# Optimization experiments

Measured on AMD Instinct MI355X. Metric: run time of the kernel, lower is better.

Reference implementation:

```python
import jax, jax.numpy as jnp
import numpy as np

DIM = 384
WS = 8        # window_size
SHIFT = 4     # shift_size
HEADS = 8
HEAD_DIM = DIM // HEADS
SCALE = HEAD_DIM ** (-0.5)
EPS = 1e-5


def layernorm(x, g, b):
    m = jnp.mean(x, axis=-1, keepdims=True)
    v = jnp.var(x, axis=-1, keepdims=True)
    return (x - m) * jax.lax.rsqrt(v + EPS) * g + b


def setup_inputs() -> dict:
    key = jax.random.key(0)
    ks = jax.random.split(key, 8)
    s = 0.02
    return {
        "x": jax.random.normal(ks[0], (8, DIM, 64, 64), dtype=jnp.float32),
        "qkv_w": jax.random.normal(ks[1], (DIM, 3 * DIM), dtype=jnp.float32) * s,
        "qkv_b": jnp.zeros((3 * DIM,), jnp.float32),
        "proj_w": jax.random.normal(ks[2], (DIM, DIM), dtype=jnp.float32) * s,
        "proj_b": jnp.zeros((DIM,), jnp.float32),
        "ln1_g": jnp.ones((DIM,), jnp.float32),
        "ln1_b": jnp.zeros((DIM,), jnp.float32),
        "ln2_g": jnp.ones((DIM,), jnp.float32),
        "ln2_b": jnp.zeros((DIM,), jnp.float32),
        "mlp_w1": jax.random.normal(ks[3], (DIM, 4 * DIM), dtype=jnp.float32) * s,
        "mlp_b1": jnp.zeros((4 * DIM,), jnp.float32),
        "mlp_w2": jax.random.normal(ks[4], (4 * DIM, DIM), dtype=jnp.float32) * s,
        "mlp_b2": jnp.zeros((DIM,), jnp.float32),
    }


def reference(x, qkv_w, qkv_b, proj_w, proj_b, ln1_g, ln1_b, ln2_g, ln2_b,
              mlp_w1, mlp_b1, mlp_w2, mlp_b2):
    B, C, H, W = x.shape
    x_skip = jnp.transpose(x, (0, 2, 3, 1))  # [B,H,W,C]
    xh = x_skip
    pad_b = (-H) % WS
    pad_r = (-W) % WS
    xh = jnp.pad(xh, ((0, 0), (0, pad_b), (0, pad_r), (0, 0)))
    Hp, Wp = xh.shape[1], xh.shape[2]
    if SHIFT > 0:
        xh = jnp.roll(xh, (-SHIFT, -SHIFT), axis=(1, 2))
    # window partition -> [B*nH*nW, WS*WS, C]
    win = xh.reshape(B, Hp // WS, WS, Wp // WS, WS, C)
    win = win.transpose(0, 1, 3, 2, 4, 5).reshape(-1, WS * WS, C)
    win = layernorm(win, ln1_g, ln1_b)
    # windowed MHA (no shift mask in original module)
    Bw, N, _ = win.shape
    qkv = (win @ qkv_w + qkv_b).reshape(Bw, N, 3, HEADS, HEAD_DIM)
    qkv = qkv.transpose(2, 0, 3, 1, 4)  # [3, Bw, H, N, d]
    q, k, v = qkv[0] * SCALE, qkv[1], qkv[2]
    attn = jax.nn.softmax(jnp.einsum('bhnd,bhmd->bhnm', q, k), axis=-1)
    out = jnp.einsum('bhnm,bhmd->bhnd', attn, v)
    out = out.transpose(0, 2, 1, 3).reshape(Bw, N, C)
    out = out @ proj_w + proj_b
    # window reverse
    xh = out.reshape(B, Hp // WS, Wp // WS, WS, WS, C)
    xh = xh.transpose(0, 1, 3, 2, 4, 5).reshape(B, Hp, Wp, C)
    if SHIFT > 0:
        xh = jnp.roll(xh, (SHIFT, SHIFT), axis=(1, 2))
    xh = xh[:, :H, :W, :] + x_skip
    h = layernorm(xh, ln2_g, ln2_b)
    h = jax.nn.gelu(h @ mlp_w1 + mlp_b1, approximate=False) @ mlp_w2 + mlp_b2
    return jnp.transpose(h, (0, 3, 1, 2))  # [B,C,H,W]
```

## Files before the change

### kernel.cpp

```cpp
#include <hip/hip_runtime.h>
#include <hip/hip_bf16.h>
#include <math.h>

#define DIM   384
#define HEADS 8
#define HD    48
#define NTOK  32768
#define NWIN  512

typedef __attribute__((ext_vector_type(8))) short bf16x8;
typedef __attribute__((ext_vector_type(8))) unsigned short u16x8;
typedef __attribute__((ext_vector_type(4))) float f32x4;

__device__ __forceinline__ float bf2f(unsigned short u) {
    unsigned int v = ((unsigned int)u) << 16;
    return __uint_as_float(v);
}
__device__ __forceinline__ unsigned short f2bf(float f) {
    unsigned int x = __float_as_uint(f);
    unsigned int r = (x + 0x7fffu + ((x >> 16) & 1u)) >> 16;
    return (unsigned short)r;
}

__device__ __forceinline__ float gelu(float v) {
    float z  = v * 0.70710678118654752f;
    float az = fabsf(z);
    float t  = __builtin_amdgcn_rcpf(1.0f + 0.47047f * az);
    float p  = t * (0.3480242f + t * (-0.0958798f + t * 0.7478556f));
    float ea = 1.0f - p * __expf(-az * az);
    float er = copysignf(ea, z);
    return 0.5f * v * (1.0f + er);
}

__device__ __forceinline__ void tok2src(int tok, int& b, int& hs, int& ws) {
    int bb  = tok >> 12;
    int win = (tok >> 6) & 63;
    int t   = tok & 63;
    int hi = win >> 3, wi = win & 7;
    int r  = t >> 3,  cc = t & 7;
    b  = bb;
    hs = (hi * 8 + r  + 4) & 63;
    ws = (wi * 8 + cc + 4) & 63;
}

__global__ __launch_bounds__(256) void k_wt4(const float* __restrict__ qkv_w,
                                             const float* __restrict__ proj_w,
                                             const float* __restrict__ w1,
                                             const float* __restrict__ w2,
                                             unsigned short* __restrict__ d0,
                                             unsigned short* __restrict__ d1,
                                             unsigned short* __restrict__ d2,
                                             unsigned short* __restrict__ d3) {
    int idx = blockIdx.x * 256 + threadIdx.x;
    const float* W; unsigned short* Wt; int K, N, loc;
    if (idx < 442368)       { W = qkv_w;  Wt = d0; K = 384;  N = 1152; loc = idx; }
    else if (idx < 589824)  { W = proj_w; Wt = d1; K = 384;  N = 384;  loc = idx - 442368; }
    else if (idx < 1179648) { W = w1;     Wt = d2; K = 384;  N = 1536; loc = idx - 589824; }
    else                    { W = w2;     Wt = d3; K = 1536; N = 384;  loc = idx - 1179648; }
    int n = loc / K, k = loc - n * K;
    Wt[loc] = f2bf(W[(size_t)k * N + n]);
}

__global__ __launch_bounds__(256) void k_ln1(const float* __restrict__ x,
                                             const float* __restrict__ g,
                                             const float* __restrict__ bt,
                                             unsigned short* __restrict__ ln1) {
    int blk = blockIdx.x;
    int b  = blk >> 6, hs = blk & 63;
    int t  = threadIdx.x;
    int w  = t & 63, cg = t >> 6;
    const float* row = x + (size_t)b * DIM * 4096 + hs * 64;

    float sum = 0.f, sq = 0.f;
    for (int i = 0; i < 96; i++) {
        int c = i * 4 + cg;
        float v = row[(size_t)c * 4096 + w];
        sum += v; sq += v * v;
    }
    __shared__ float red[2][4][64];
    __shared__ float mean_s[64], rstd_s[64];
    red[0][cg][w] = sum; red[1][cg][w] = sq;
    __syncthreads();
    if (t < 64) {
        float s  = red[0][0][t] + red[0][1][t] + red[0][2][t] + red[0][3][t];
        float q2 = red[1][0][t] + red[1][1][t] + red[1][2][t] + red[1][3][t];
        float mean = s * (1.0f / DIM);
        float var  = q2 * (1.0f / DIM) - mean * mean;
        mean_s[t] = mean;
        rstd_s[t] = rsqrtf(var + 1e-5f);
    }
    __syncthreads();

    int wp = t >> 2, seg = t & 3;
    int hr = (hs + 60) & 63, wr = (wp + 60) & 63;
    int tok = ((b * 8 + (hr >> 3)) * 8 + (wr >> 3)) * 64 + (hr & 7) * 8 + (wr & 7);

    __shared__ __align__(16) unsigned short tile[64][72];
    for (int chunk = 0; chunk < 6; chunk++) {
        float mean = mean_s[w], rstd = rstd_s[w];
        #pragma unroll
        for (int it = 0; it < 16; it++) {
            int cl = it * 4 + cg;
            int c  = chunk * 64 + cl;
            float v = row[(size_t)c * 4096 + w];
            tile[w][cl] = f2bf((v - mean) * rstd * g[c] + bt[c]);
        }
        __syncthreads();
        u16x8 v0 = *(const u16x8*)&tile[wp][seg * 16];
        u16x8 v1 = *(const u16x8*)&tile[wp][seg * 16 + 8];
        unsigned short* op = ln1 + (size_t)tok * DIM + chunk * 64 + seg * 16;
        *(u16x8*)op = v0;
        *(u16x8*)(op + 8) = v1;
        __syncthreads();
    }
}

template <int EPI>
__global__ __launch_bounds__(256) void k_gemm_mfma(
        const unsigned short* __restrict__ A,
        const unsigned short* __restrict__ Bt,
        const float* __restrict__ bias,
        void* __restrict__ Cout,
        const float* __restrict__ xres,
        int N, int K, int GX) {
    __shared__ __align__(16) unsigned short SH[24576];
    int tid  = threadIdx.x;
    int lane = tid & 63;
    int wave = tid >> 6;
    int wm = wave >> 1, wn = wave & 1;
    int quad = lane >> 4, l15 = lane & 15;

    int l   = blockIdx.x;
    int xcd = l & 7;
    int r_  = l >> 3;
    int bx  = r_ % GX;
    int by  = (r_ / GX) * 8 + xcd;
    int m0 = by * 128, n0 = bx * 128;

    const unsigned short* gA0 = A  + (size_t)(m0 +      lane) * K + wave * 8;
    const unsigned short* gA1 = A  + (size_t)(m0 + 64 + lane) * K + wave * 8;
    const unsigned short* gB0 = Bt + (size_t)(n0 +      lane) * K + wave * 8;
    const unsigned short* gB1 = Bt + (size_t)(n0 + 64 + lane) * K + wave * 8;

    auto stage = [&](int buf) {
        __builtin_amdgcn_global_load_lds(
            (const __attribute__((address_space(1))) void*)gA0,
            (__attribute__((address_space(3))) void*)&SH[buf * 4096 + wave * 1024],
            16, 0, 0);
        __builtin_amdgcn_global_load_lds(
            (const __attribute__((address_space(1))) void*)gA1,
            (__attribute__((address_space(3))) void*)&SH[buf * 4096 + wave * 1024 + 512],
            16, 0, 0);
        __builtin_amdgcn_global_load_lds(
            (const __attribute__((address_space(1))) void*)gB0,
            (__attribute__((address_space(3))) void*)&SH[12288 + buf * 4096 + wave * 1024],
            16, 0, 0);
        __builtin_amdgcn_global_load_lds(
            (const __attribute__((address_space(1))) void*)gB1,
            (__attribute__((address_space(3))) void*)&SH[12288 + buf * 4096 + wave * 1024 + 512],
            16, 0, 0);
        gA0 += 32; gA1 += 32; gB0 += 32; gB1 += 32;
    };

    f32x4 acc[4][4] = {};
    int nsteps = K >> 5;

    stage(0);
    stage(1);
    int cur = 0, nxt = 2;
    for (int t = 0; t < nsteps; ++t) {
        __builtin_amdgcn_s_barrier();
        if (t + 2 < nsteps) {
            stage(nxt);
            if (++nxt == 3) nxt = 0;
            asm volatile("s_waitcnt vmcnt(8)" ::: "memory");
        } else if (t + 2 == nsteps) {
            asm volatile("s_waitcnt vmcnt(4)" ::: "memory");
        } else {
            asm volatile("s_waitcnt vmcnt(0)" ::: "memory");
        }
        __builtin_amdgcn_s_barrier();

        bf16x8 af[4], bfr[4];
        #pragma unroll
        for (int r = 0; r < 4; r++)
            af[r] = *(const bf16x8*)&SH[cur * 4096 + (quad * 128 + wm * 64 + r * 16 + l15) * 8];
        #pragma unroll
        for (int r2 = 0; r2 < 4; r2++)
            bfr[r2] = *(const bf16x8*)&SH[12288 + cur * 4096 + (quad * 128 + wn * 64 + r2 * 16 + l15) * 8];
        #pragma unroll
        for (int r = 0; r < 4; r++)
            #pragma unroll
            for (int r2 = 0; r2 < 4; r2++)
                acc[r][r2] = __builtin_amdgcn_mfma_f32_16x16x32_bf16(
                                 af[r], bfr[r2], acc[r][r2], 0, 0, 0);
        if (++cur == 3) cur = 0;
    }

    if (EPI == 2 || EPI == 3) {
        #pragma unroll
        for (int r2 = 0; r2 < 4; r2++) {
            int n = n0 + wn * 64 + r2 * 16 + l15;
            float bn = bias[n];
            #pragma unroll
            for (int r = 0; r < 4; r++) {
                #pragma unroll
                for (int reg = 0; reg < 4; reg++) {
                    int m = m0 + wm * 64 + r * 16 + quad * 4 + reg;
                    float v = acc[r][r2][reg] + bn;
                    if (EPI == 2) {
                        int b, hs, ws_;
                        tok2src(m, b, hs, ws_);
                        v += xres[(((size_t)b * DIM + n) * 64 + hs) * 64 + ws_];
                    }
                    ((float*)Cout)[(size_t)m * N + n] = v;
                }
            }
        }
    } else {
        __syncthreads();
        #pragma unroll
        for (int r2 = 0; r2 < 4; r2++) {
            int col = wn * 64 + r2 * 16 + l15;
            float bn = bias[n0 + col];
            #pragma unroll
            for (int r = 0; r < 4; r++) {
                int row0 = wm * 64 + r * 16 + quad * 4;
                #pragma unroll
                for (int reg = 0; reg < 4; reg++) {
                    int row = row0 + reg;
                    float v = acc[r][r2][reg] + bn;
                    if (EPI == 1) v = gelu(v);
                    SH[(row * 136 + col) ^ (((row >> 3) & 1) << 4)] = f2bf(v);
                }
            }
        }
        __syncthreads();
        #pragma unroll
        for (int i = 0; i < 8; i++) {
            int chunk = tid + i * 256;
            int m = chunk >> 4, nc = chunk & 15;
            int idx = (m * 136 + nc * 8) ^ (((m >> 3) & 1) << 4);
            u16x8 v = *(const u16x8*)&SH[idx];
            if (EPI == 4) {
                int n = n0 + nc * 8;
                int qi  = n / 384;
                int rem = n - qi * 384;
                int hh  = rem / 48;
                int d   = rem - hh * 48;
                *(u16x8*)&((unsigned short*)Cout)[((size_t)(qi * 8 + hh) * NTOK + m0 + m) * 48 + d] = v;
            } else {
                *(u16x8*)&((unsigned short*)Cout)[(size_t)(m0 + m) * N + n0 + nc * 8] = v;
            }
        }
    }
}

__global__ __launch_bounds__(256) void k_attn_mfma(
        const unsigned short* __restrict__ qkvh,
        unsigned short* __restrict__ attn) {
    __shared__ __align__(16) unsigned short lds[4][8064];
    int tid  = threadIdx.x;
    int lane = tid & 63;
    int wave = tid >> 6;
    int quad = lane >> 4, l15 = lane & 15;
    int win  = blockIdx.x;
    int tok0 = win * 64;
    unsigned short* VT = &lds[wave][0];
    unsigned short* P  = &lds[wave][3456];
    const float scale = 0.14433756729740643f;

    for (int hi = 0; hi < 2; hi++) {
        int h = wave + hi * 4;
        const unsigned short* qb = qkvh + ((size_t)(0 * 8 + h) * NTOK + tok0) * 48;
        const unsigned short* kb = qkvh + ((size_t)(1 * 8 + h) * NTOK + tok0) * 48;
        const unsigned short* vb = qkvh + ((size_t)(2 * 8 + h) * NTOK + tok0) * 48;

        #pragma unroll
        for (int i = 0; i < 6; i++) {
            u16x8 v = *(const u16x8*)&vb[lane * 48 + i * 8];
            #pragma unroll
            for (int j = 0; j < 8; j++)
                VT[(i * 8 + j) * 72 + lane] = v[j];
        }

        bf16x8 kf[4][2];
        #pragma unroll
        for (int ni = 0; ni < 4; ni++) {
            kf[ni][0] = *(const bf16x8*)&kb[(ni * 16 + l15) * 48 + quad * 8];
            bf16x8 z = {};
            if (quad < 2)
                z = *(const bf16x8*)&kb[(ni * 16 + l15) * 48 + 32 + quad * 8];
            kf[ni][1] = z;
        }

        f32x4 sacc[4][4] = {};
        #pragma unroll
        for (int mi = 0; mi < 4; mi++) {
            bf16x8 qf0 = *(const bf16x8*)&qb[(mi * 16 + l15) * 48 + quad * 8];
            bf16x8 qf1 = {};
            if (quad < 2)
                qf1 = *(const bf16x8*)&qb[(mi * 16 + l15) * 48 + 32 + quad * 8];
            #pragma unroll
            for (int ni = 0; ni < 4; ni++) {
                sacc[mi][ni] = __builtin_amdgcn_mfma_f32_16x16x32_bf16(qf0, kf[ni][0], sacc[mi][ni], 0, 0, 0);
                sacc[mi][ni] = __builtin_amdgcn_mfma_f32_16x16x32_bf16(qf1, kf[ni][1], sacc[mi][ni], 0, 0, 0);
            }
        }

        #pragma unroll
        for (int mi = 0; mi < 4; mi++) {
            #pragma unroll
            for (int reg = 0; reg < 4; reg++) {
                float s0 = sacc[mi][0][reg] * scale;
                float s1 = sacc[mi][1][reg] * scale;
                float s2 = sacc[mi][2][reg] * scale;
                float s3 = sacc[mi][3][reg] * scale;
                float mx = fmaxf(fmaxf(s0, s1), fmaxf(s2, s3));
                #pragma unroll
                for (int off = 1; off < 16; off <<= 1)
                    mx = fmaxf(mx, __shfl_xor(mx, off));
                float e0 = __expf(s0 - mx);
                float e1 = __expf(s1 - mx);
                float e2 = __expf(s2 - mx);
                float e3 = __expf(s3 - mx);
                float sm = e0 + e1 + e2 + e3;
                #pragma unroll
                for (int off = 1; off < 16; off <<= 1)
                    sm += __shfl_xor(sm, off);
                float inv = 1.0f / sm;
                int row = mi * 16 + quad * 4 + reg;
                P[row * 72 +  0 + l15] = f2bf(e0 * inv);
                P[row * 72 + 16 + l15] = f2bf(e1 * inv);
                P[row * 72 + 32 + l15] = f2bf(e2 * inv);
                P[row * 72 + 48 + l15] = f2bf(e3 * inv);
            }
        }

        bf16x8 vf[3][2];
        #pragma unroll
        for (int ni = 0; ni < 3; ni++)
            #pragma unroll
            for (int kt = 0; kt < 2; kt++)
                vf[ni][kt] = *(const bf16x8*)&VT[(ni * 16 + l15) * 72 + kt * 32 + quad * 8];

        #pragma unroll
        for (int mi = 0; mi < 4; mi++) {
            bf16x8 pf0 = *(const bf16x8*)&P[(mi * 16 + l15) * 72 + quad * 8];
            bf16x8 pf1 = *(const bf16x8*)&P[(mi * 16 + l15) * 72 + 32 + quad * 8];
            f32x4 o[3] = {};
            #pragma unroll
            for (int ni = 0; ni < 3; ni++) {
                o[ni] = __builtin_amdgcn_mfma_f32_16x16x32_bf16(pf0, vf[ni][0], o[ni], 0, 0, 0);
                o[ni] = __builtin_amdgcn_mfma_f32_16x16x32_bf16(pf1, vf[ni][1], o[ni], 0, 0, 0);
            }
            #pragma unroll
            for (int ni = 0; ni < 3; ni++)
                #pragma unroll
                for (int reg = 0; reg < 4; reg++) {
                    int tok = tok0 + mi * 16 + quad * 4 + reg;
                    attn[(size_t)tok * DIM + h * HD + ni * 16 + l15] = f2bf(o[ni][reg]);
                }
        }
    }
}

__global__ __launch_bounds__(64) void k_ln2(const float* __restrict__ y,
                                            const float* __restrict__ g,
                                            const float* __restrict__ bt,
                                            unsigned short* __restrict__ out) {
    int tok = blockIdx.x;
    int t   = threadIdx.x;
    const float* row = y + (size_t)tok * DIM;
    float v[6];
    float sum = 0.f, sq = 0.f;
    #pragma unroll
    for (int i = 0; i < 6; i++) {
        v[i] = row[i * 64 + t];
        sum += v[i]; sq += v[i] * v[i];
    }
    #pragma unroll
    for (int o = 32; o > 0; o >>= 1) {
        sum += __shfl_xor(sum, o, 64);
        sq  += __shfl_xor(sq, o, 64);
    }
    float mean = sum * (1.0f / DIM);
    float var  = sq * (1.0f / DIM) - mean * mean;
    float rstd = rsqrtf(var + 1e-5f);
    unsigned short* orow = out + (size_t)tok * DIM;
    #pragma unroll
    for (int i = 0; i < 6; i++) {
        int c = i * 64 + t;
        orow[c] = f2bf((v[i] - mean) * rstd * g[c] + bt[c]);
    }
}

__global__ __launch_bounds__(256) void k_out(const float* __restrict__ hbuf,
                                             float* __restrict__ out) {
    int bh = blockIdx.x;
    int b = bh >> 6, h = bh & 63;
    int t = threadIdx.x;
    __shared__ float T[64][193];
    int hh = (h + 60) & 63;
    int hi = hh >> 3, r = hh & 7;
    for (int half = 0; half < 2; half++) {
        int c0 = half * 192;
        for (int idx = t; idx < 64 * 192; idx += 256) {
            int w = idx / 192;
            int c = idx - w * 192;
            int ww = (w + 60) & 63;
            int wi = ww >> 3, cc2 = ww & 7;
            int tok = ((b * 8 + hi) * 8 + wi) * 64 + r * 8 + cc2;
            T[w][c] = hbuf[(size_t)tok * DIM + c0 + c];
        }
        __syncthreads();
        for (int idx = t; idx < 64 * 192; idx += 256) {
            int cc = idx >> 6;
            int w  = idx & 63;
            out[(((size_t)b * DIM + c0 + cc) * 64 + h) * 64 + w] = T[w][cc];
        }
        __syncthreads();
    }
}

extern "C" void kernel_launch(void* const* d_in, const int* in_sizes, int n_in,
                              void* d_out, int out_size, void* d_ws, size_t ws_size,
                              hipStream_t stream) {
    const float* x      = (const float*)d_in[0];
    const float* qkv_w  = (const float*)d_in[1];
    const float* qkv_b  = (const float*)d_in[2];
    const float* proj_w = (const float*)d_in[3];
    const float* proj_b = (const float*)d_in[4];
    const float* ln1_g  = (const float*)d_in[5];
    const float* ln1_b  = (const float*)d_in[6];
    const float* ln2_g  = (const float*)d_in[7];
    const float* ln2_b  = (const float*)d_in[8];
    const float* w1     = (const float*)d_in[9];
    const float* b1     = (const float*)d_in[10];
    const float* w2     = (const float*)d_in[11];
    const float* b2     = (const float*)d_in[12];

    char* ws = (char*)d_ws;
    unsigned short* qkv_wt  = (unsigned short*)(ws + 0);
    unsigned short* proj_wt = (unsigned short*)(ws + 884736);
    unsigned short* w1t     = (unsigned short*)(ws + 1179648);
    unsigned short* w2t     = (unsigned short*)(ws + 2359296);
    unsigned short* ln1     = (unsigned short*)(ws + 4194304);
    unsigned short* qkv     = (unsigned short*)(ws + 29360128);
    unsigned short* attn    = (unsigned short*)(ws + 104857600);
    float*          y       = (float*)(ws + 130023424);
    unsigned short* ln2     = ln1;
    unsigned short* mid     = qkv;
    float*          hbuf    = y;

    k_wt4<<<6912, 256, 0, stream>>>(qkv_w, proj_w, w1, w2, qkv_wt, proj_wt, w1t, w2t);
    k_ln1<<<512, 256, 0, stream>>>(x, ln1_g, ln1_b, ln1);
    k_gemm_mfma<4><<<9 * 256, 256, 0, stream>>>(ln1, qkv_wt, qkv_b, qkv, nullptr, 1152, 384, 9);
    k_attn_mfma<<<NWIN, 256, 0, stream>>>(qkv, attn);
    k_gemm_mfma<2><<<3 * 256, 256, 0, stream>>>(attn, proj_wt, proj_b, y, x, 384, 384, 3);
    k_ln2<<<NTOK, 64, 0, stream>>>(y, ln2_g, ln2_b, ln2);
    k_gemm_mfma<1><<<12 * 256, 256, 0, stream>>>(ln2, w1t, b1, mid, nullptr, 1536, 384, 12);
    k_gemm_mfma<3><<<3 * 256, 256, 0, stream>>>(mid, w2t, b2, hbuf, nullptr, 384, 1536, 3);
    k_out<<<NWIN, 256, 0, stream>>>(hbuf, (float*)d_out);
}
```

Measured before the change: 492.0 us.

## Tile weight transpose through LDS, drop GEMM triple buffering, halve epilogue LDS

The weight-transpose kernel becomes a 64x64 tiled transpose through shared memory, so both its reads and writes are coalesced instead of doing strided per-element reads. The GEMM drops its three-stage global_load_lds pipeline for a single buffer with two syncthreads per K step. Its epilogue is split into two 64-row halves so LDS per block shrinks from 48KB to about 17KB, which allows higher occupancy. f2bf now uses the native __bf16 conversion. Losing the prefetch exposes global-load latency in every K step, which has to be hidden by more resident blocks instead.

```diff
diff --git a/kernel.cpp b/kernel.cpp
--- a/kernel.cpp
+++ b/kernel.cpp
@@ -17,9 +17,8 @@
     return __uint_as_float(v);
 }
 __device__ __forceinline__ unsigned short f2bf(float f) {
-    unsigned int x = __float_as_uint(f);
-    unsigned int r = (x + 0x7fffu + ((x >> 16) & 1u)) >> 16;
-    return (unsigned short)r;
+    __bf16 b = (__bf16)f;
+    return __builtin_bit_cast(unsigned short, b);
 }
 
 __device__ __forceinline__ float gelu(float v) {
@@ -51,14 +50,28 @@
                                              unsigned short* __restrict__ d1,
                                              unsigned short* __restrict__ d2,
                                              unsigned short* __restrict__ d3) {
-    int idx = blockIdx.x * 256 + threadIdx.x;
-    const float* W; unsigned short* Wt; int K, N, loc;
-    if (idx < 442368)       { W = qkv_w;  Wt = d0; K = 384;  N = 1152; loc = idx; }
-    else if (idx < 589824)  { W = proj_w; Wt = d1; K = 384;  N = 384;  loc = idx - 442368; }
-    else if (idx < 1179648) { W = w1;     Wt = d2; K = 384;  N = 1536; loc = idx - 589824; }
-    else                    { W = w2;     Wt = d3; K = 1536; N = 384;  loc = idx - 1179648; }
-    int n = loc / K, k = loc - n * K;
-    Wt[loc] = f2bf(W[(size_t)k * N + n]);
+    __shared__ unsigned short T[64][66];
+    int b = blockIdx.x;
+    const float* W; unsigned short* Wt; int K, N, lt;
+    if (b < 108)      { W = qkv_w;  Wt = d0; K = 384;  N = 1152; lt = b; }
+    else if (b < 144) { W = proj_w; Wt = d1; K = 384;  N = 384;  lt = b - 108; }
+    else if (b < 288) { W = w1;     Wt = d2; K = 384;  N = 1536; lt = b - 144; }
+    else              { W = w2;     Wt = d3; K = 1536; N = 384;  lt = b - 288; }
+    int tn = N >> 6;
+    int k0 = (lt / tn) << 6, n0 = (lt % tn) << 6;
+    int t  = threadIdx.x;
+    int cl = t & 63, rw = t >> 6;
+    #pragma unroll
+    for (int p = 0; p < 16; p++) {
+        int kk = p * 4 + rw;
+        T[cl][kk] = f2bf(W[(size_t)(k0 + kk) * N + n0 + cl]);
+    }
+    __syncthreads();
+    #pragma unroll
+    for (int p = 0; p < 16; p++) {
+        int nn = p * 4 + rw;
+        Wt[(size_t)(n0 + nn) * K + k0 + cl] = T[nn][cl];
+    }
 }
 
 __global__ __launch_bounds__(256) void k_ln1(const float* __restrict__ x,
@@ -123,7 +136,7 @@
         void* __restrict__ Cout,
         const float* __restrict__ xres,
         int N, int K, int GX) {
-    __shared__ __align__(16) unsigned short SH[24576];
+    __shared__ __align__(16) unsigned short SH[8704];
     int tid  = threadIdx.x;
     int lane = tid & 63;
     int wave = tid >> 6;
@@ -142,59 +155,43 @@
     const unsigned short* gB0 = Bt + (size_t)(n0 +      lane) * K + wave * 8;
     const unsigned short* gB1 = Bt + (size_t)(n0 + 64 + lane) * K + wave * 8;
 
-    auto stage = [&](int buf) {
+    f32x4 acc[4][4] = {};
+    int nsteps = K >> 5;
+
+    for (int t = 0; t < nsteps; ++t) {
         __builtin_amdgcn_global_load_lds(
             (const __attribute__((address_space(1))) void*)gA0,
-            (__attribute__((address_space(3))) void*)&SH[buf * 4096 + wave * 1024],
+            (__attribute__((address_space(3))) void*)&SH[wave * 1024],
             16, 0, 0);
         __builtin_amdgcn_global_load_lds(
             (const __attribute__((address_space(1))) void*)gA1,
-            (__attribute__((address_space(3))) void*)&SH[buf * 4096 + wave * 1024 + 512],
+            (__attribute__((address_space(3))) void*)&SH[wave * 1024 + 512],
             16, 0, 0);
         __builtin_amdgcn_global_load_lds(
             (const __attribute__((address_space(1))) void*)gB0,
-            (__attribute__((address_space(3))) void*)&SH[12288 + buf * 4096 + wave * 1024],
+            (__attribute__((address_space(3))) void*)&SH[4096 + wave * 1024],
             16, 0, 0);
         __builtin_amdgcn_global_load_lds(
             (const __attribute__((address_space(1))) void*)gB1,
-            (__attribute__((address_space(3))) void*)&SH[12288 + buf * 4096 + wave * 1024 + 512],
+            (__attribute__((address_space(3))) void*)&SH[4096 + wave * 1024 + 512],
             16, 0, 0);
         gA0 += 32; gA1 += 32; gB0 += 32; gB1 += 32;
-    };
-
-    f32x4 acc[4][4] = {};
-    int nsteps = K >> 5;
-
-    stage(0);
-    stage(1);
-    int cur = 0, nxt = 2;
-    for (int t = 0; t < nsteps; ++t) {
-        __builtin_amdgcn_s_barrier();
-        if (t + 2 < nsteps) {
-            stage(nxt);
-            if (++nxt == 3) nxt = 0;
-            asm volatile("s_waitcnt vmcnt(8)" ::: "memory");
-        } else if (t + 2 == nsteps) {
-            asm volatile("s_waitcnt vmcnt(4)" ::: "memory");
-        } else {
-            asm volatile("s_waitcnt vmcnt(0)" ::: "memory");
-        }
-        __builtin_amdgcn_s_barrier();
+        __syncthreads();
 
         bf16x8 af[4], bfr[4];
         #pragma unroll
         for (int r = 0; r < 4; r++)
-            af[r] = *(const bf16x8*)&SH[cur * 4096 + (quad * 128 + wm * 64 + r * 16 + l15) * 8];
+            af[r] = *(const bf16x8*)&SH[(quad * 128 + wm * 64 + r * 16 + l15) * 8];
         #pragma unroll
         for (int r2 = 0; r2 < 4; r2++)
-            bfr[r2] = *(const bf16x8*)&SH[12288 + cur * 4096 + (quad * 128 + wn * 64 + r2 * 16 + l15) * 8];
+            bfr[r2] = *(const bf16x8*)&SH[4096 + (quad * 128 + wn * 64 + r2 * 16 + l15) * 8];
         #pragma unroll
         for (int r = 0; r < 4; r++)
             #pragma unroll
             for (int r2 = 0; r2 < 4; r2++)
                 acc[r][r2] = __builtin_amdgcn_mfma_f32_16x16x32_bf16(
                                  af[r], bfr[r2], acc[r][r2], 0, 0, 0);
-        if (++cur == 3) cur = 0;
+        __syncthreads();
     }
 
     if (EPI == 2 || EPI == 3) {
@@ -218,40 +215,46 @@
             }
         }
     } else {
-        __syncthreads();
-        #pragma unroll
-        for (int r2 = 0; r2 < 4; r2++) {
-            int col = wn * 64 + r2 * 16 + l15;
-            float bn = bias[n0 + col];
-            #pragma unroll
-            for (int r = 0; r < 4; r++) {
-                int row0 = wm * 64 + r * 16 + quad * 4;
+        #pragma unroll
+        for (int half = 0; half < 2; half++) {
+            if (wm == half) {
                 #pragma unroll
-                for (int reg = 0; reg < 4; reg++) {
-                    int row = row0 + reg;
-                    float v = acc[r][r2][reg] + bn;
-                    if (EPI == 1) v = gelu(v);
-                    SH[(row * 136 + col) ^ (((row >> 3) & 1) << 4)] = f2bf(v);
+                for (int r2 = 0; r2 < 4; r2++) {
+                    int col = wn * 64 + r2 * 16 + l15;
+                    float bn = bias[n0 + col];
+                    #pragma unroll
+                    for (int r = 0; r < 4; r++) {
+                        int row0 = r * 16 + quad * 4;
+                        #pragma unroll
+                        for (int reg = 0; reg < 4; reg++) {
+                            int row = row0 + reg;
+                            float v = acc[r][r2][reg] + bn;
+                            if (EPI == 1) v = gelu(v);
+                            SH[(row * 136 + col) ^ (((row >> 3) & 1) << 4)] = f2bf(v);
+                        }
+                    }
                 }
             }
-        }
-        __syncthreads();
-        #pragma unroll
-        for (int i = 0; i < 8; i++) {
-            int chunk = tid + i * 256;
-            int m = chunk >> 4, nc = chunk & 15;
-            int idx = (m * 136 + nc * 8) ^ (((m >> 3) & 1) << 4);
-            u16x8 v = *(const u16x8*)&SH[idx];
-            if (EPI == 4) {
-                int n = n0 + nc * 8;
-                int qi  = n / 384;
-                int rem = n - qi * 384;
-                int hh  = rem / 48;
-                int d   = rem - hh * 48;
-                *(u16x8*)&((unsigned short*)Cout)[((size_t)(qi * 8 + hh) * NTOK + m0 + m) * 48 + d] = v;
-            } else {
-                *(u16x8*)&((unsigned short*)Cout)[(size_t)(m0 + m) * N + n0 + nc * 8] = v;
-            }
+            __syncthreads();
+            #pragma unroll
+            for (int i = 0; i < 4; i++) {
+                int chunk = tid + i * 256;
+                int ml = chunk >> 4, nc = chunk & 15;
+                int idx = (ml * 136 + nc * 8) ^ (((ml >> 3) & 1) << 4);
+                u16x8 v = *(const u16x8*)&SH[idx];
+                int m = m0 + half * 64 + ml;
+                if (EPI == 4) {
+                    int n = n0 + nc * 8;
+                    int qi  = n / 384;
+                    int rem = n - qi * 384;
+                    int hh  = rem / 48;
+                    int d   = rem - hh * 48;
+                    *(u16x8*)&((unsigned short*)Cout)[((size_t)(qi * 8 + hh) * NTOK + m) * 48 + d] = v;
+                } else {
+                    *(u16x8*)&((unsigned short*)Cout)[(size_t)m * N + n0 + nc * 8] = v;
+                }
+            }
+            __syncthreads();
         }
     }
 }
@@ -453,7 +456,7 @@
     unsigned short* mid     = qkv;
     float*          hbuf    = y;
 
-    k_wt4<<<6912, 256, 0, stream>>>(qkv_w, proj_w, w1, w2, qkv_wt, proj_wt, w1t, w2t);
+    k_wt4<<<432, 256, 0, stream>>>(qkv_w, proj_w, w1, w2, qkv_wt, proj_wt, w1t, w2t);
     k_ln1<<<512, 256, 0, stream>>>(x, ln1_g, ln1_b, ln1);
     k_gemm_mfma<4><<<9 * 256, 256, 0, stream>>>(ln1, qkv_wt, qkv_b, qkv, nullptr, 1152, 384, 9);
     k_attn_mfma<<<NWIN, 256, 0, stream>>>(qkv, attn);
```

Result: slower. 556.4 us (+13.1%).
